# Optimization experiments

Measured on AMD Instinct MI355X. Metric: run time of the kernel, lower is better.

## Reference

```python
import jax, jax.numpy as jnp
import numpy as np
import math

B, N, E, H, D = 8, 1024, 1024, 16, 64  # batch, node_cnt, embedding_dim, head_num, qkv_dim
SQRT_E, SQRT_D, CLIP = 32.0, 8.0, 10.0
MAX_PERIOD = 10000.0


def setup_inputs() -> dict:
    key = jax.random.key(0)
    ks = jax.random.split(key, 16)
    s = 0.03  # weight scale keeps tanh/softmax in a sane range
    return {
        "t": jax.random.uniform(ks[0], (B,), jnp.float32),
        "encoded_jobs": jax.random.normal(ks[1], (B, N, E), jnp.float32) * 0.5,
        "xt": jax.random.uniform(ks[2], (B, N, N), jnp.float32),
        "Wq": jax.random.normal(ks[3], (H * D, E), jnp.float32) * s,
        "Wk": jax.random.normal(ks[4], (H * D, E), jnp.float32) * s,
        "Wv": jax.random.normal(ks[5], (H * D, E), jnp.float32) * s,
        "Wc": jax.random.normal(ks[6], (E, H * D), jnp.float32) * s,
        "bc": jnp.zeros((E,), jnp.float32),
        "conv_w": jax.random.normal(ks[7], (2, 2), jnp.float32) * 0.5,  # 1x1 Conv2d(2,2)
        "conv_b": jnp.zeros((2,), jnp.float32),
        "tW1": jax.random.normal(ks[8], (E // 2, E), jnp.float32) * s,
        "tb1": jnp.zeros((E // 2,), jnp.float32),
        "tW2": jax.random.normal(ks[9], (E, E // 2), jnp.float32) * s,
        "tb2": jnp.zeros((E,), jnp.float32),
    }


def _timestep_embedding(t):
    half = E // 2
    freqs = jnp.exp(-math.log(MAX_PERIOD) * jnp.arange(half, dtype=jnp.float32) / half)
    args = t[:, None] * freqs[None, :]               # [B, E/2]
    return jnp.concatenate([jnp.cos(args), jnp.sin(args)], axis=-1)  # [B, E]


def reference(t, encoded_jobs, xt, Wq, Wk, Wv, Wc, bc, conv_w, conv_b, tW1, tb1, tW2, tb2):
    # time embedding MLP
    t_emb = jax.nn.relu(_timestep_embedding(t) @ tW1.T + tb1) @ tW2.T + tb2  # [B, E]

    def heads(W):
        return (encoded_jobs @ W.T).reshape(B, N, H, D).transpose(0, 2, 1, 3)  # [B,H,N,D]

    q, k, v = heads(Wq), heads(Wk), heads(Wv)
    attn = jax.nn.softmax(jnp.einsum('bhnd,bhmd->bhnm', q, k) / SQRT_D, axis=-1)
    out = jnp.einsum('bhnm,bhmd->bhnd', attn, v)
    out_concat = out.transpose(0, 2, 1, 3).reshape(B, N, H * D)
    mh = out_concat @ Wc.T + bc + t_emb[:, None, :]          # [B,N,E]

    # single-head score against encoded_jobs^T, scaled + tanh-clipped
    score = jnp.einsum('bne,bme->bnm', mh, encoded_jobs) / SQRT_E
    score_clipped = CLIP * jnp.tanh(score)

    stacked = jnp.stack([score_clipped, xt], axis=1)         # [B,2,N,N]
    conv_out = jnp.einsum('oi,binm->bonm', conv_w, stacked) + conv_b[None, :, None, None]
    return jax.nn.softmax(conv_out.transpose(0, 2, 3, 1), axis=3)  # [B,N,N,2]
```

## Files before the change

kernel.cpp:

```cpp
#include <hip/hip_runtime.h>
#include <hip/hip_bf16.h>
#include <math.h>

#define B_ 8
#define N_ 1024
#define E_ 1024
#define H_ 16
#define D_ 64

typedef __attribute__((ext_vector_type(8))) short short8;
typedef __attribute__((ext_vector_type(4))) float f32x4;

static __device__ __forceinline__ unsigned short f2bf(float f) {
    __hip_bfloat16 h = __float2bfloat16(f);
    return __builtin_bit_cast(unsigned short, h);
}
static __device__ __forceinline__ unsigned int cvtpk_bf16(float a, float b) {
    unsigned int r;
    asm("v_cvt_pk_bf16_f32 %0, %1, %2" : "=v"(r) : "v"(a), "v"(b));
    return r;
}
static __device__ __forceinline__ void gld_lds16(const void* g, void* l) {
    __builtin_amdgcn_global_load_lds(
        (const __attribute__((address_space(1))) unsigned int*)g,
        (__attribute__((address_space(3))) unsigned int*)l, 16, 0, 0);
}

__global__ __launch_bounds__(256) void cvt_multi(
    const float* __restrict__ s0, const float* __restrict__ s1,
    const float* __restrict__ s2, const float* __restrict__ s3,
    const float* __restrict__ s4,
    unsigned short* __restrict__ d0, unsigned short* __restrict__ d1,
    unsigned short* __restrict__ d2, unsigned short* __restrict__ d3,
    unsigned short* __restrict__ d4, int nbig, int nsmall)
{
    const int z = blockIdx.y;
    const float* s; unsigned short* d; int n;
    switch (z) {
        case 0: s = s0; d = d0; n = nbig; break;
        case 1: s = s1; d = d1; n = nsmall; break;
        case 2: s = s2; d = d2; n = nsmall; break;
        case 3: s = s3; d = d3; n = nsmall; break;
        default: s = s4; d = d4; n = nsmall; break;
    }
    int i = (blockIdx.x * 256 + threadIdx.x) * 4;
    if (i >= n) return;
    float4 v = *(const float4*)(s + i);
    *(ushort4*)(d + i) = make_ushort4(f2bf(v.x), f2bf(v.y), f2bf(v.z), f2bf(v.w));
}

__global__ __launch_bounds__(256) void temb1_kernel(
    const float* __restrict__ t, const float* __restrict__ tW1,
    const float* __restrict__ tb1, float* __restrict__ h1T)
{
    const int wv = threadIdx.x >> 6, lane = threadIdx.x & 63;
    const int j = blockIdx.x * 4 + wv;
    float tv[8];
#pragma unroll
    for (int b = 0; b < 8; ++b) tv[b] = t[b];
    const float* w = tW1 + j * 1024;
    float acc[8];
#pragma unroll
    for (int b = 0; b < 8; ++b) acc[b] = 0.f;
    const float kLog = 9.210340371976184f;
    for (int e = lane; e < 1024; e += 64) {
        float we = w[e];
        int ef = e & 511;
        float freq = __expf(-kLog * (float)ef * (1.0f / 512.0f));
        if (e < 512) {
#pragma unroll
            for (int b = 0; b < 8; ++b) acc[b] = fmaf(we, __cosf(tv[b] * freq), acc[b]);
        } else {
#pragma unroll
            for (int b = 0; b < 8; ++b) acc[b] = fmaf(we, __sinf(tv[b] * freq), acc[b]);
        }
    }
#pragma unroll
    for (int off = 32; off > 0; off >>= 1)
#pragma unroll
        for (int b = 0; b < 8; ++b) acc[b] += __shfl_xor(acc[b], off, 64);
    if (lane == 0) {
        float bias = tb1[j];
#pragma unroll
        for (int b = 0; b < 8; ++b) h1T[j * 8 + b] = fmaxf(acc[b] + bias, 0.f);
    }
}

__global__ __launch_bounds__(256) void temb2_kernel(
    const float* __restrict__ h1T, const float* __restrict__ tW2,
    const float* __restrict__ tb2, float* __restrict__ temb)
{
    const int wv = threadIdx.x >> 6, lane = threadIdx.x & 63;
    const int e2 = blockIdx.x * 4 + wv;
    const float* w = tW2 + e2 * 512;
    float acc[8];
#pragma unroll
    for (int b = 0; b < 8; ++b) acc[b] = 0.f;
    for (int j = lane; j < 512; j += 64) {
        float wv_ = w[j];
        const float* hp = h1T + j * 8;
#pragma unroll
        for (int b = 0; b < 8; ++b) acc[b] = fmaf(hp[b], wv_, acc[b]);
    }
#pragma unroll
    for (int off = 32; off > 0; off >>= 1)
#pragma unroll
        for (int b = 0; b < 8; ++b) acc[b] += __shfl_xor(acc[b], off, 64);
    if (lane == 0) {
        float bias = tb2[e2];
#pragma unroll
        for (int b = 0; b < 8; ++b) temb[b * 1024 + e2] = acc[b] + bias;
    }
}

static __device__ __forceinline__ void gemm_loop(
    const unsigned short* __restrict__ A, const unsigned short* __restrict__ Bm,
    int m0, int n0, int K,
    unsigned short* As0, unsigned short* As1,
    unsigned short* Bs0, unsigned short* Bs1,
    f32x4 acc[4][4])
{
    const int tid = threadIdx.x;
    const int wave = tid >> 6, lane = tid & 63;
    const int wm = wave >> 1, wn = wave & 1;
    const int sr = lane >> 2, sc = (lane & 3) * 8;
    const unsigned short* Ag0 = A + (size_t)(m0 + wave * 16 + sr) * K + sc;
    const unsigned short* Ag1 = A + (size_t)(m0 + 64 + wave * 16 + sr) * K + sc;
    const unsigned short* Bg0 = Bm + (size_t)(n0 + wave * 16 + sr) * K + sc;
    const unsigned short* Bg1 = Bm + (size_t)(n0 + 64 + wave * 16 + sr) * K + sc;

    const f32x4 zero = {0.f, 0.f, 0.f, 0.f};
#pragma unroll
    for (int i = 0; i < 4; ++i)
#pragma unroll
        for (int j = 0; j < 4; ++j) acc[i][j] = zero;

    gld_lds16(Ag0, As0 + wave * 512);
    gld_lds16(Ag1, As0 + (wave + 4) * 512);
    gld_lds16(Bg0, Bs0 + wave * 512);
    gld_lds16(Bg1, Bs0 + (wave + 4) * 512);
    __syncthreads();

    const int fr = lane & 15, fq = (lane >> 4) * 8;
    int cur = 0;
    for (int k0 = 0; k0 < K; k0 += 32) {
        const unsigned short* sA = cur ? As1 : As0;
        const unsigned short* sB = cur ? Bs1 : Bs0;
        unsigned short* dA = cur ? As0 : As1;
        unsigned short* dB = cur ? Bs0 : Bs1;
        if (k0 + 32 < K) {
            gld_lds16(Ag0 + k0 + 32, dA + wave * 512);
            gld_lds16(Ag1 + k0 + 32, dA + (wave + 4) * 512);
            gld_lds16(Bg0 + k0 + 32, dB + wave * 512);
            gld_lds16(Bg1 + k0 + 32, dB + (wave + 4) * 512);
        }
        short8 af[4], bf[4];
#pragma unroll
        for (int i = 0; i < 4; ++i) {
            af[i] = *(const short8*)&sA[(wm * 64 + i * 16 + fr) * 32 + fq];
            bf[i] = *(const short8*)&sB[(wn * 64 + i * 16 + fr) * 32 + fq];
        }
#pragma unroll
        for (int i = 0; i < 4; ++i)
#pragma unroll
            for (int j = 0; j < 4; ++j)
                acc[i][j] = __builtin_amdgcn_mfma_f32_16x16x32_bf16(
                    af[i], bf[j], acc[i][j], 0, 0, 0);
        __syncthreads();
        cur ^= 1;
    }
}

static __device__ __forceinline__ void gemm_loop64(
    const unsigned short* __restrict__ A, const unsigned short* __restrict__ Bm,
    int m0, int n0, int K,
    unsigned short* As0, unsigned short* As1,
    unsigned short* Bs0, unsigned short* Bs1,
    f32x4 acc[2][4])
{
    const int tid = threadIdx.x;
    const int wave = tid >> 6, lane = tid & 63;
    const int wm = wave >> 1, wn = wave & 1;
    const int sr = lane >> 2, sc = (lane & 3) * 8;
    const unsigned short* Ag0 = A + (size_t)(m0 + wave * 16 + sr) * K + sc;
    const unsigned short* Bg0 = Bm + (size_t)(n0 + wave * 16 + sr) * K + sc;
    const unsigned short* Bg1 = Bm + (size_t)(n0 + 64 + wave * 16 + sr) * K + sc;

    const f32x4 zero = {0.f, 0.f, 0.f, 0.f};
#pragma unroll
    for (int i = 0; i < 2; ++i)
#pragma unroll
        for (int j = 0; j < 4; ++j) acc[i][j] = zero;

    gld_lds16(Ag0, As0 + wave * 512);
    gld_lds16(Bg0, Bs0 + wave * 512);
    gld_lds16(Bg1, Bs0 + (wave + 4) * 512);
    __syncthreads();

    const int fr = lane & 15, fq = (lane >> 4) * 8;
    int cur = 0;
    for (int k0 = 0; k0 < K; k0 += 32) {
        const unsigned short* sA = cur ? As1 : As0;
        const unsigned short* sB = cur ? Bs1 : Bs0;
        unsigned short* dA = cur ? As0 : As1;
        unsigned short* dB = cur ? Bs0 : Bs1;
        if (k0 + 32 < K) {
            gld_lds16(Ag0 + k0 + 32, dA + wave * 512);
            gld_lds16(Bg0 + k0 + 32, dB + wave * 512);
            gld_lds16(Bg1 + k0 + 32, dB + (wave + 4) * 512);
        }
        short8 af[2], bf[4];
#pragma unroll
        for (int i = 0; i < 2; ++i)
            af[i] = *(const short8*)&sA[(wm * 32 + i * 16 + fr) * 32 + fq];
#pragma unroll
        for (int j = 0; j < 4; ++j)
            bf[j] = *(const short8*)&sB[(wn * 64 + j * 16 + fr) * 32 + fq];
#pragma unroll
        for (int i = 0; i < 2; ++i)
#pragma unroll
            for (int j = 0; j < 4; ++j)
                acc[i][j] = __builtin_amdgcn_mfma_f32_16x16x32_bf16(
                    af[i], bf[j], acc[i][j], 0, 0, 0);
        __syncthreads();
        cur ^= 1;
    }
}

__global__ __launch_bounds__(256) void qkv_gemm(
    const unsigned short* __restrict__ A,
    const unsigned short* __restrict__ W0, const unsigned short* __restrict__ W1,
    const unsigned short* __restrict__ W2,
    unsigned short* __restrict__ C0, unsigned short* __restrict__ C1,
    unsigned short* __restrict__ C2)
{
    __shared__ unsigned short As0[128 * 32], As1[128 * 32];
    __shared__ unsigned short Bs0[128 * 32], Bs1[128 * 32];
    const int orig = blockIdx.x;
    const int sw = (orig & 7) * 192 + (orig >> 3);
    const int z = sw / 512, r = sw & 511;
    const int m0 = (r >> 3) * 128, n0 = (r & 7) * 128;
    const unsigned short* W = z == 0 ? W0 : (z == 1 ? W1 : W2);
    unsigned short* C = z == 0 ? C0 : (z == 1 ? C1 : C2);

    f32x4 acc[4][4];
    gemm_loop(A, W, m0, n0, 1024, As0, As1, Bs0, Bs1, acc);

    const int lane = threadIdx.x & 63, wave = threadIdx.x >> 6;
    const int wm = wave >> 1, wn = wave & 1;
    const int fr = lane & 15, fq4 = (lane >> 4) * 4;
#pragma unroll
    for (int i = 0; i < 4; ++i) {
        int row = m0 + wm * 64 + i * 16 + fq4;
#pragma unroll
        for (int j = 0; j < 4; ++j) {
            int col = n0 + wn * 64 + j * 16 + fr;
#pragma unroll
            for (int rr = 0; rr < 4; ++rr)
                C[(size_t)(row + rr) * 1024 + col] = f2bf(acc[i][j][rr]);
        }
    }
}

__global__ __launch_bounds__(256) void outproj_gemm(
    const unsigned short* __restrict__ A, const unsigned short* __restrict__ Bm,
    unsigned short* __restrict__ C,
    const float* __restrict__ bias, const float* __restrict__ temb)
{
    __shared__ unsigned short As0[64 * 32], As1[64 * 32];
    __shared__ unsigned short Bs0[128 * 32], Bs1[128 * 32];
    const int orig = blockIdx.x;
    const int sw = (orig & 7) * 128 + (orig >> 3);
    const int mt = sw >> 3, n0 = (sw & 7) * 128;
    const int m0 = mt * 64;

    f32x4 acc[2][4];
    gemm_loop64(A, Bm, m0, n0, 1024, As0, As1, Bs0, Bs1, acc);

    const int lane = threadIdx.x & 63, wave = threadIdx.x >> 6;
    const int wm = wave >> 1, wn = wave & 1;
    const int fr = lane & 15, fq4 = (lane >> 4) * 4;
    const int bb = m0 >> 10;
#pragma unroll
    for (int i = 0; i < 2; ++i) {
        int row = m0 + wm * 32 + i * 16 + fq4;
#pragma unroll
        for (int j = 0; j < 4; ++j) {
            int col = n0 + wn * 64 + j * 16 + fr;
            float epi = bias[col] + temb[bb * 1024 + col];
#pragma unroll
            for (int rr = 0; rr < 4; ++rr)
                C[(size_t)(row + rr) * 1024 + col] = f2bf(acc[i][j][rr] + epi);
        }
    }
}

__global__ __launch_bounds__(256, 2) void attn_mfma(
    const unsigned short* __restrict__ Q, const unsigned short* __restrict__ K,
    const unsigned short* __restrict__ V, unsigned short* __restrict__ O)
{
    __shared__ __align__(16) unsigned short Ks[64 * 72];
    __shared__ __align__(16) unsigned short Vts[80 * 72];
    const int tid = threadIdx.x;
    const int wq = tid >> 6, lane = tid & 63;
    const int lo = lane & 15, hi = lane >> 4;
    const int id = blockIdx.x;
    const int sw = (id & 7) * 64 + (id >> 3);
    const int q0 = (sw & 3) * 256;
    const int h = (sw >> 2) & 15, b = sw >> 6;
    const size_t base = ((size_t)b * N_) * 1024 + h * 64;

    for (int i = tid; i < 16 * 64; i += 256) {
        int rr = i >> 6, cc = i & 63;
        Vts[(64 + rr) * 72 + cc] = (rr == 0) ? (unsigned short)0x3F80 : (unsigned short)0;
    }
    __syncthreads();
    short8 vb4[2];
#pragma unroll
    for (int k2 = 0; k2 < 2; ++k2)
        vb4[k2] = *(const short8*)&Vts[(64 + lo) * 72 + hi * 8 + k2 * 32];

    short8 aq[4][2];
#pragma unroll
    for (int qt = 0; qt < 4; ++qt)
#pragma unroll
        for (int ks = 0; ks < 2; ++ks)
            aq[qt][ks] = *(const short8*)(Q + base +
                (size_t)(q0 + wq * 64 + qt * 16 + lo) * 1024 + hi * 8 + ks * 32);

    f32x4 o_[4][5];
    const f32x4 zero = {0.f, 0.f, 0.f, 0.f};
#pragma unroll
    for (int qt = 0; qt < 4; ++qt)
#pragma unroll
        for (int db = 0; db < 5; ++db) o_[qt][db] = zero;

    const int kr = tid >> 2, ku = (tid & 3) * 16;
    const unsigned short* Kg = K + base + (size_t)kr * 1024 + ku;
    const int vkv = (tid & 31) * 2, vd = (tid >> 5) * 8;
    const int scol = (vkv & 0x23) | ((vkv & 0x0C) << 1) | ((vkv & 0x10) >> 2);
    const unsigned short* Vg = V + base + (size_t)vkv * 1024 + vd;

    short8 kl0 = *(const short8*)(Kg);
    short8 kl1 = *(const short8*)(Kg + 8);
    short8 vla = *(const short8*)(Vg);
    short8 vlb = *(const short8*)(Vg + 1024);

    const float cexp = 0.1803368801111204f;

    for (int kt = 0; kt < N_; kt += 64) {
        __syncthreads();
        *(short8*)&Ks[kr * 72 + ku] = kl0;
        *(short8*)&Ks[kr * 72 + ku + 8] = kl1;
#pragma unroll
        for (int i = 0; i < 8; ++i) {
            unsigned int pv = (unsigned int)(unsigned short)vla[i] |
                              ((unsigned int)(unsigned short)vlb[i] << 16);
            *(unsigned int*)&Vts[(vd + i) * 72 + scol] = pv;
        }
        __syncthreads();
        if (kt + 64 < N_) {
            kl0 = *(const short8*)(Kg + (size_t)(kt + 64) * 1024);
            kl1 = *(const short8*)(Kg + (size_t)(kt + 64) * 1024 + 8);
            vla = *(const short8*)(Vg + (size_t)(kt + 64) * 1024);
            vlb = *(const short8*)(Vg + (size_t)(kt + 64) * 1024 + 1024);
        }

        short8 kb[4][2], vb[4][2];
#pragma unroll
        for (int jk = 0; jk < 4; ++jk)
#pragma unroll
            for (int ks = 0; ks < 2; ++ks)
                kb[jk][ks] = *(const short8*)&Ks[(16 * jk + lo) * 72 + hi * 8 + ks * 32];
#pragma unroll
        for (int db = 0; db < 4; ++db)
#pragma unroll
            for (int k2 = 0; k2 < 2; ++k2)
                vb[db][k2] = *(const short8*)&Vts[(16 * db + lo) * 72 +
                                                  hi * 8 + k2 * 32];

#pragma unroll
        for (int qt = 0; qt < 4; ++qt) {
            f32x4 s[4];
            __builtin_amdgcn_s_setprio(1);
#pragma unroll
            for (int jk = 0; jk < 4; ++jk) {
                s[jk] = __builtin_amdgcn_mfma_f32_16x16x32_bf16(
                    kb[jk][0], aq[qt][0], zero, 0, 0, 0);
                s[jk] = __builtin_amdgcn_mfma_f32_16x16x32_bf16(
                    kb[jk][1], aq[qt][1], s[jk], 0, 0, 0);
            }
            __builtin_amdgcn_s_setprio(0);
#pragma unroll
            for (int jk = 0; jk < 4; ++jk)
#pragma unroll
                for (int rr = 0; rr < 4; ++rr)
                    s[jk][rr] = exp2f(s[jk][rr] * cexp);
            unsigned int pw[8];
#pragma unroll
            for (int jk = 0; jk < 4; ++jk) {
                pw[2 * jk] = cvtpk_bf16(s[jk][0], s[jk][1]);
                pw[2 * jk + 1] = cvtpk_bf16(s[jk][2], s[jk][3]);
            }
            uint4 pa0 = make_uint4(pw[0], pw[1], pw[2], pw[3]);
            uint4 pa1 = make_uint4(pw[4], pw[5], pw[6], pw[7]);
            short8 pA = __builtin_bit_cast(short8, pa0);
            short8 pB = __builtin_bit_cast(short8, pa1);

            __builtin_amdgcn_s_setprio(1);
#pragma unroll
            for (int db = 0; db < 4; ++db) {
                o_[qt][db] = __builtin_amdgcn_mfma_f32_16x16x32_bf16(
                    vb[db][0], pA, o_[qt][db], 0, 0, 0);
                o_[qt][db] = __builtin_amdgcn_mfma_f32_16x16x32_bf16(
                    vb[db][1], pB, o_[qt][db], 0, 0, 0);
            }
            o_[qt][4] = __builtin_amdgcn_mfma_f32_16x16x32_bf16(
                vb4[0], pA, o_[qt][4], 0, 0, 0);
            o_[qt][4] = __builtin_amdgcn_mfma_f32_16x16x32_bf16(
                vb4[1], pB, o_[qt][4], 0, 0, 0);
            __builtin_amdgcn_s_setprio(0);
        }
    }

#pragma unroll
    for (int qt = 0; qt < 4; ++qt) {
        float lsum = __shfl(o_[qt][4][0], lo, 64);
        float inv = 1.f / lsum;
        const size_t rb = base + (size_t)(q0 + wq * 64 + qt * 16 + lo) * 1024;
#pragma unroll
        for (int db = 0; db < 4; ++db) {
            *(ushort4*)(O + rb + 16 * db + 4 * hi) = make_ushort4(
                f2bf(o_[qt][db][0] * inv), f2bf(o_[qt][db][1] * inv),
                f2bf(o_[qt][db][2] * inv), f2bf(o_[qt][db][3] * inv));
        }
    }
}

__global__ __launch_bounds__(256) void score_bf16(
    const unsigned short* __restrict__ MH, const unsigned short* __restrict__ EJ,
    const float* __restrict__ xt, const float* __restrict__ convw,
    const float* __restrict__ convb, float* __restrict__ out)
{
    __shared__ unsigned short As0[64 * 32], As1[64 * 32];
    __shared__ unsigned short Bs0[128 * 32], Bs1[128 * 32];
    const int orig = blockIdx.x;
    const int sw = (orig & 7) * 128 + (orig >> 3);
    const int bz = sw >> 7;
    const int m0 = ((sw >> 3) & 15) * 64, n0 = (sw & 7) * 128;
    const unsigned short* A = MH + (size_t)bz * N_ * E_;
    const unsigned short* Bm = EJ + (size_t)bz * N_ * E_;

    f32x4 acc[2][4];
    gemm_loop64(A, Bm, m0, n0, 1024, As0, As1, Bs0, Bs1, acc);

    const int lane = threadIdx.x & 63, wave = threadIdx.x >> 6;
    const int wm = wave >> 1, wn = wave & 1;
    const int fr = lane & 15, fq4 = (lane >> 4) * 4;
    const float w00 = convw[0], w01 = convw[1], w10 = convw[2], w11 = convw[3];
    const float cb0 = convb[0], cb1 = convb[1];
    const float L2E = 1.4426950408889634f;
    const float kT = -2.f * L2E * 0.03125f;
#pragma unroll
    for (int i = 0; i < 2; ++i) {
#pragma unroll
        for (int rr = 0; rr < 4; ++rr) {
            int row = m0 + wm * 32 + i * 16 + fq4 + rr;
            const float* xrow = xt + ((size_t)bz * N_ + row) * N_;
            float2* orow = (float2*)(out + (((size_t)bz * N_ + row) * N_) * 2);
#pragma unroll
            for (int j = 0; j < 4; ++j) {
                int col = n0 + wn * 64 + j * 16 + fr;
                float e = exp2f(acc[i][j][rr] * kT);
                float sc_ = fmaf(20.f, 1.f / (1.f + e), -10.f);
                float x = xrow[col];
                float c0 = fmaf(w00, sc_, fmaf(w01, x, cb0));
                float c1 = fmaf(w10, sc_, fmaf(w11, x, cb1));
                float e1 = exp2f((c1 - c0) * L2E);
                float o0 = 1.f / (1.f + e1);
                orow[col] = make_float2(o0, 1.f - o0);
            }
        }
    }
}

extern "C" void kernel_launch(void* const* d_in, const int* in_sizes, int n_in,
                              void* d_out, int out_size, void* d_ws, size_t ws_size,
                              hipStream_t stream)
{
    (void)in_sizes; (void)n_in; (void)out_size; (void)ws_size;
    const float* t     = (const float*)d_in[0];
    const float* ej    = (const float*)d_in[1];
    const float* xt    = (const float*)d_in[2];
    const float* Wq    = (const float*)d_in[3];
    const float* Wk    = (const float*)d_in[4];
    const float* Wv    = (const float*)d_in[5];
    const float* Wc    = (const float*)d_in[6];
    const float* bc    = (const float*)d_in[7];
    const float* convw = (const float*)d_in[8];
    const float* convb = (const float*)d_in[9];
    const float* tW1   = (const float*)d_in[10];
    const float* tb1   = (const float*)d_in[11];
    const float* tW2   = (const float*)d_in[12];
    const float* tb2   = (const float*)d_in[13];
    float* out = (float*)d_out;

    const size_t SZ = (size_t)B_ * N_ * 1024;
    float* ws = (float*)d_ws;
    float* temb = ws;
    float* h1T  = ws + 8192;
    unsigned short* ej_bf = (unsigned short*)(ws + 8192 + 4096);
    unsigned short* MH_bf = ej_bf + SZ;
    unsigned short* Wq_bf = MH_bf + SZ;
    unsigned short* Wk_bf = Wq_bf + (size_t)E_ * 1024;
    unsigned short* Wv_bf = Wk_bf + (size_t)E_ * 1024;
    unsigned short* Wc_bf = Wv_bf + (size_t)E_ * 1024;

    unsigned short* Qb = (unsigned short*)d_out;
    unsigned short* Kb = Qb + SZ;
    unsigned short* Vb = Kb + SZ;
    unsigned short* Ob = Vb + SZ;

    cvt_multi<<<dim3(8192, 5), dim3(256), 0, stream>>>(
        ej, Wq, Wk, Wv, Wc, ej_bf, Wq_bf, Wk_bf, Wv_bf, Wc_bf,
        (int)SZ, E_ * 1024);
    temb1_kernel<<<dim3(128), dim3(256), 0, stream>>>(t, tW1, tb1, h1T);
    temb2_kernel<<<dim3(256), dim3(256), 0, stream>>>(h1T, tW2, tb2, temb);

    dim3 gblk(256);
    qkv_gemm<<<dim3(1536), gblk, 0, stream>>>(
        ej_bf, Wq_bf, Wk_bf, Wv_bf, Qb, Kb, Vb);

    attn_mfma<<<dim3(512), gblk, 0, stream>>>(Qb, Kb, Vb, Ob);

    outproj_gemm<<<dim3(1024), gblk, 0, stream>>>(Ob, Wc_bf, MH_bf, bc, temb);

    score_bf16<<<dim3(1024), gblk, 0, stream>>>(
        MH_bf, ej_bf, xt, convw, convb, out);
}
```

Measured before the change: 215.0 us.

## Triple-buffer LDS staging in GEMM loops with vmcnt-based waits

Switches the shared GEMM main loops (QKV, output projection, score) from double to triple buffering of the LDS tiles. Global-to-LDS loads are issued two k-steps ahead, and the full __syncthreads is replaced by a partial s_waitcnt vmcnt plus s_barrier, so one stage of loads stays in flight across the barrier. The aim is to hide global load latency behind MFMA work. The cost is 50% more LDS per block, which can lower occupancy, and correctness now depends on hand-counted vmcnt values.

```diff
diff --git a/kernel.cpp b/kernel.cpp
--- a/kernel.cpp
+++ b/kernel.cpp
@@ -113,11 +113,21 @@
     }
 }
 
+static __device__ __forceinline__ void stage128(
+    const unsigned short* Ag0, const unsigned short* Ag1,
+    const unsigned short* Bg0, const unsigned short* Bg1, int koff,
+    unsigned short* dA, unsigned short* dB, int wave)
+{
+    gld_lds16(Ag0 + koff, dA + wave * 512);
+    gld_lds16(Ag1 + koff, dA + (wave + 4) * 512);
+    gld_lds16(Bg0 + koff, dB + wave * 512);
+    gld_lds16(Bg1 + koff, dB + (wave + 4) * 512);
+}
+
 static __device__ __forceinline__ void gemm_loop(
     const unsigned short* __restrict__ A, const unsigned short* __restrict__ Bm,
     int m0, int n0, int K,
-    unsigned short* As0, unsigned short* As1,
-    unsigned short* Bs0, unsigned short* Bs1,
+    unsigned short* As, unsigned short* Bs,
     f32x4 acc[4][4])
 {
     const int tid = threadIdx.x;
@@ -135,30 +145,23 @@
 #pragma unroll
         for (int j = 0; j < 4; ++j) acc[i][j] = zero;
 
-    gld_lds16(Ag0, As0 + wave * 512);
-    gld_lds16(Ag1, As0 + (wave + 4) * 512);
-    gld_lds16(Bg0, Bs0 + wave * 512);
-    gld_lds16(Bg1, Bs0 + (wave + 4) * 512);
-    __syncthreads();
+    unsigned short *a0 = As, *a1 = As + 4096, *a2 = As + 8192;
+    unsigned short *b0 = Bs, *b1 = Bs + 4096, *b2 = Bs + 8192;
+    stage128(Ag0, Ag1, Bg0, Bg1, 0, a0, b0, wave);
+    stage128(Ag0, Ag1, Bg0, Bg1, 32, a1, b1, wave);
+    asm volatile("s_waitcnt vmcnt(4)" ::: "memory");
+    __builtin_amdgcn_s_barrier();
 
     const int fr = lane & 15, fq = (lane >> 4) * 8;
-    int cur = 0;
     for (int k0 = 0; k0 < K; k0 += 32) {
-        const unsigned short* sA = cur ? As1 : As0;
-        const unsigned short* sB = cur ? Bs1 : Bs0;
-        unsigned short* dA = cur ? As0 : As1;
-        unsigned short* dB = cur ? Bs0 : Bs1;
-        if (k0 + 32 < K) {
-            gld_lds16(Ag0 + k0 + 32, dA + wave * 512);
-            gld_lds16(Ag1 + k0 + 32, dA + (wave + 4) * 512);
-            gld_lds16(Bg0 + k0 + 32, dB + wave * 512);
-            gld_lds16(Bg1 + k0 + 32, dB + (wave + 4) * 512);
-        }
+        __builtin_amdgcn_sched_barrier(0);
+        if (k0 + 64 < K)
+            stage128(Ag0, Ag1, Bg0, Bg1, k0 + 64, a2, b2, wave);
         short8 af[4], bf[4];
 #pragma unroll
         for (int i = 0; i < 4; ++i) {
-            af[i] = *(const short8*)&sA[(wm * 64 + i * 16 + fr) * 32 + fq];
-            bf[i] = *(const short8*)&sB[(wn * 64 + i * 16 + fr) * 32 + fq];
+            af[i] = *(const short8*)&a0[(wm * 64 + i * 16 + fr) * 32 + fq];
+            bf[i] = *(const short8*)&b0[(wn * 64 + i * 16 + fr) * 32 + fq];
         }
 #pragma unroll
         for (int i = 0; i < 4; ++i)
@@ -166,16 +169,33 @@
             for (int j = 0; j < 4; ++j)
                 acc[i][j] = __builtin_amdgcn_mfma_f32_16x16x32_bf16(
                     af[i], bf[j], acc[i][j], 0, 0, 0);
-        __syncthreads();
-        cur ^= 1;
-    }
+        if (k0 + 32 < K) {
+            if (k0 + 64 < K)
+                asm volatile("s_waitcnt vmcnt(4)" ::: "memory");
+            else
+                asm volatile("s_waitcnt vmcnt(0)" ::: "memory");
+            __builtin_amdgcn_s_barrier();
+        }
+        unsigned short* tp;
+        tp = a0; a0 = a1; a1 = a2; a2 = tp;
+        tp = b0; b0 = b1; b1 = b2; b2 = tp;
+    }
+}
+
+static __device__ __forceinline__ void stage64(
+    const unsigned short* Ag0, const unsigned short* Bg0,
+    const unsigned short* Bg1, int koff,
+    unsigned short* dA, unsigned short* dB, int wave)
+{
+    gld_lds16(Ag0 + koff, dA + wave * 512);
+    gld_lds16(Bg0 + koff, dB + wave * 512);
+    gld_lds16(Bg1 + koff, dB + (wave + 4) * 512);
 }
 
 static __device__ __forceinline__ void gemm_loop64(
     const unsigned short* __restrict__ A, const unsigned short* __restrict__ Bm,
     int m0, int n0, int K,
-    unsigned short* As0, unsigned short* As1,
-    unsigned short* Bs0, unsigned short* Bs1,
+    unsigned short* As, unsigned short* Bs,
     f32x4 acc[2][4])
 {
     const int tid = threadIdx.x;
@@ -192,38 +212,41 @@
 #pragma unroll
         for (int j = 0; j < 4; ++j) acc[i][j] = zero;
 
-    gld_lds16(Ag0, As0 + wave * 512);
-    gld_lds16(Bg0, Bs0 + wave * 512);
-    gld_lds16(Bg1, Bs0 + (wave + 4) * 512);
-    __syncthreads();
+    unsigned short *a0 = As, *a1 = As + 2048, *a2 = As + 4096;
+    unsigned short *b0 = Bs, *b1 = Bs + 4096, *b2 = Bs + 8192;
+    stage64(Ag0, Bg0, Bg1, 0, a0, b0, wave);
+    stage64(Ag0, Bg0, Bg1, 32, a1, b1, wave);
+    asm volatile("s_waitcnt vmcnt(3)" ::: "memory");
+    __builtin_amdgcn_s_barrier();
 
     const int fr = lane & 15, fq = (lane >> 4) * 8;
-    int cur = 0;
     for (int k0 = 0; k0 < K; k0 += 32) {
-        const unsigned short* sA = cur ? As1 : As0;
-        const unsigned short* sB = cur ? Bs1 : Bs0;
-        unsigned short* dA = cur ? As0 : As1;
-        unsigned short* dB = cur ? Bs0 : Bs1;
-        if (k0 + 32 < K) {
-            gld_lds16(Ag0 + k0 + 32, dA + wave * 512);
-            gld_lds16(Bg0 + k0 + 32, dB + wave * 512);
-            gld_lds16(Bg1 + k0 + 32, dB + (wave + 4) * 512);
-        }
+        __builtin_amdgcn_sched_barrier(0);
+        if (k0 + 64 < K)
+            stage64(Ag0, Bg0, Bg1, k0 + 64, a2, b2, wave);
         short8 af[2], bf[4];
 #pragma unroll
         for (int i = 0; i < 2; ++i)
-            af[i] = *(const short8*)&sA[(wm * 32 + i * 16 + fr) * 32 + fq];
+            af[i] = *(const short8*)&a0[(wm * 32 + i * 16 + fr) * 32 + fq];
 #pragma unroll
         for (int j = 0; j < 4; ++j)
-            bf[j] = *(const short8*)&sB[(wn * 64 + j * 16 + fr) * 32 + fq];
+            bf[j] = *(const short8*)&b0[(wn * 64 + j * 16 + fr) * 32 + fq];
 #pragma unroll
         for (int i = 0; i < 2; ++i)
 #pragma unroll
             for (int j = 0; j < 4; ++j)
                 acc[i][j] = __builtin_amdgcn_mfma_f32_16x16x32_bf16(
                     af[i], bf[j], acc[i][j], 0, 0, 0);
-        __syncthreads();
-        cur ^= 1;
+        if (k0 + 32 < K) {
+            if (k0 + 64 < K)
+                asm volatile("s_waitcnt vmcnt(3)" ::: "memory");
+            else
+                asm volatile("s_waitcnt vmcnt(0)" ::: "memory");
+            __builtin_amdgcn_s_barrier();
+        }
+        unsigned short* tp;
+        tp = a0; a0 = a1; a1 = a2; a2 = tp;
+        tp = b0; b0 = b1; b1 = b2; b2 = tp;
     }
 }
 
@@ -234,8 +257,8 @@
     unsigned short* __restrict__ C0, unsigned short* __restrict__ C1,
     unsigned short* __restrict__ C2)
 {
-    __shared__ unsigned short As0[128 * 32], As1[128 * 32];
-    __shared__ unsigned short Bs0[128 * 32], Bs1[128 * 32];
+    __shared__ unsigned short As[3 * 4096];
+    __shared__ unsigned short Bs[3 * 4096];
     const int orig = blockIdx.x;
     const int sw = (orig & 7) * 192 + (orig >> 3);
     const int z = sw / 512, r = sw & 511;
@@ -244,7 +267,7 @@
     unsigned short* C = z == 0 ? C0 : (z == 1 ? C1 : C2);
 
     f32x4 acc[4][4];
-    gemm_loop(A, W, m0, n0, 1024, As0, As1, Bs0, Bs1, acc);
+    gemm_loop(A, W, m0, n0, 1024, As, Bs, acc);
 
     const int lane = threadIdx.x & 63, wave = threadIdx.x >> 6;
     const int wm = wave >> 1, wn = wave & 1;
@@ -267,15 +290,15 @@
     unsigned short* __restrict__ C,
     const float* __restrict__ bias, const float* __restrict__ temb)
 {
-    __shared__ unsigned short As0[64 * 32], As1[64 * 32];
-    __shared__ unsigned short Bs0[128 * 32], Bs1[128 * 32];
+    __shared__ unsigned short As[3 * 2048];
+    __shared__ unsigned short Bs[3 * 4096];
     const int orig = blockIdx.x;
     const int sw = (orig & 7) * 128 + (orig >> 3);
     const int mt = sw >> 3, n0 = (sw & 7) * 128;
     const int m0 = mt * 64;
 
     f32x4 acc[2][4];
-    gemm_loop64(A, Bm, m0, n0, 1024, As0, As1, Bs0, Bs1, acc);
+    gemm_loop64(A, Bm, m0, n0, 1024, As, Bs, acc);
 
     const int lane = threadIdx.x & 63, wave = threadIdx.x >> 6;
     const int wm = wave >> 1, wn = wave & 1;
@@ -442,8 +465,8 @@
     const float* __restrict__ xt, const float* __restrict__ convw,
     const float* __restrict__ convb, float* __restrict__ out)
 {
-    __shared__ unsigned short As0[64 * 32], As1[64 * 32];
-    __shared__ unsigned short Bs0[128 * 32], Bs1[128 * 32];
+    __shared__ unsigned short As[3 * 2048];
+    __shared__ unsigned short Bs[3 * 4096];
     const int orig = blockIdx.x;
     const int sw = (orig & 7) * 128 + (orig >> 3);
     const int bz = sw >> 7;
@@ -452,7 +475,7 @@
     const unsigned short* Bm = EJ + (size_t)bz * N_ * E_;
 
     f32x4 acc[2][4];
-    gemm_loop64(A, Bm, m0, n0, 1024, As0, As1, Bs0, Bs1, acc);
+    gemm_loop64(A, Bm, m0, n0, 1024, As, Bs, acc);
 
     const int lane = threadIdx.x & 63, wave = threadIdx.x >> 6;
     const int wm = wave >> 1, wn = wave & 1;
```

Measured after the change: 232.3 us. 8.0% more time.
